# Kernel tuning notes

Hardware: AMD Instinct MI355X
Metric: run time of the kernel (lower is better)

Reference implementation:

```python
import jax, jax.numpy as jnp
import numpy as np

B, S, D_IN, D_ATT = 8, 2048, 512, 512

def setup_inputs() -> dict:
    key = jax.random.key(0)
    ks = jax.random.split(key, 7)
    sc = 1.0 / np.sqrt(D_IN)
    return {
        "x": jax.random.normal(ks[0], (B, S, D_IN), dtype=jnp.float32),
        "Wq": jax.random.uniform(ks[1], (D_IN, D_ATT), jnp.float32, -sc, sc),
        "bq": jax.random.uniform(ks[2], (D_ATT,), jnp.float32, -sc, sc),
        "Wk": jax.random.uniform(ks[3], (D_IN, D_ATT), jnp.float32, -sc, sc),
        "bk": jax.random.uniform(ks[4], (D_ATT,), jnp.float32, -sc, sc),
        "Wv": jax.random.uniform(ks[5], (D_IN, D_ATT), jnp.float32, -sc, sc),
        "bv": jax.random.uniform(ks[6], (D_ATT,), jnp.float32, -sc, sc),
    }

def reference(x, Wq, bq, Wk, bk, Wv, bv):
    # Linear projections: [B, S, D_att]
    q = jnp.einsum("bsd,de->bse", x, Wq) + bq
    k = jnp.einsum("bsd,de->bse", x, Wk) + bk
    v = jnp.einsum("bsd,de->bse", x, Wv) + bv
    # Full scores matrix [B, S, S]; note: NO 1/sqrt(d) scaling in original.
    scores = jnp.einsum("bqe,bke->bqk", q, k)
    attn = jax.nn.softmax(scores, axis=-1)
    return jnp.einsum("bqk,bke->bqe", attn, v)
```

## Files before the change

### kernel.cpp

```cpp
#include <hip/hip_runtime.h>
#include <cstdint>
#include <cstddef>


#define SEQ 2048
#define DIM 512
#define NB 8
#define BSZ (NB * SEQ)
#define KT 64
#define NT (SEQ / KT)

typedef __attribute__((ext_vector_type(8))) _Float16 half8;
typedef __attribute__((ext_vector_type(4))) float f32x4;

__device__ __forceinline__ unsigned short f2h(float f) {
  _Float16 h = (_Float16)f;
  return __builtin_bit_cast(unsigned short, h);
}
__device__ __forceinline__ half8 ld_frag(const unsigned short* p) {
  return *(const half8*)(const void*)p;
}
__device__ __forceinline__ void gl_lds16(const unsigned short* g, unsigned short* l) {
  __builtin_amdgcn_global_load_lds(
      (__attribute__((address_space(1))) void*)g,
      (__attribute__((address_space(3))) void*)l, 16, 0, 0);
}
__device__ __forceinline__ void bar_vm0() {
  asm volatile("s_waitcnt vmcnt(0)\ns_barrier" ::: "memory");
}
__device__ __forceinline__ void bar_lgkm_vm0() {
  asm volatile("s_waitcnt lgkmcnt(0) vmcnt(0)\ns_barrier" ::: "memory");
}

__global__ __launch_bounds__(256) void cvt_x_kernel(
    const float* __restrict__ X, unsigned short* __restrict__ xh)
{
  size_t i0 = ((size_t)blockIdx.x * 256 + threadIdx.x) * 8;
  float4 a = *(const float4*)&X[i0];
  float4 b = *(const float4*)&X[i0 + 4];
  ushort4 o0; o0.x = f2h(a.x); o0.y = f2h(a.y); o0.z = f2h(a.z); o0.w = f2h(a.w);
  ushort4 o1; o1.x = f2h(b.x); o1.y = f2h(b.y); o1.z = f2h(b.z); o1.w = f2h(b.w);
  *(ushort4*)&xh[i0] = o0;
  *(ushort4*)&xh[i0 + 4] = o1;
}

__global__ __launch_bounds__(256) void cvt_w_kernel(
    const float* __restrict__ Wq, const float* __restrict__ Wk,
    const float* __restrict__ Wv, unsigned short* __restrict__ Wt)
{
  const int z = blockIdx.z;
  const float* W = (z == 0) ? Wq : (z == 1) ? Wk : Wv;
  unsigned short* out = Wt + (size_t)z * DIM * DIM;
  const int k0 = blockIdx.x * 64, n0 = blockIdx.y * 64;
  const int t = threadIdx.x;
  __shared__ unsigned short tl[64 * 72];
#pragma unroll
  for (int i = 0; i < 4; i++) {
    int f = t + 256 * i;
    int kr = f >> 4, c4 = (f & 15) * 4;
    float4 v = *(const float4*)&W[(size_t)(k0 + kr) * DIM + n0 + c4];
    tl[(c4 + 0) * 72 + kr] = f2h(v.x);
    tl[(c4 + 1) * 72 + kr] = f2h(v.y);
    tl[(c4 + 2) * 72 + kr] = f2h(v.z);
    tl[(c4 + 3) * 72 + kr] = f2h(v.w);
  }
  __syncthreads();
#pragma unroll
  for (int i = 0; i < 2; i++) {
    int f = t + 256 * i;
    int nr = f >> 3, k8 = (f & 7) * 8;
    *(uint4*)&out[(size_t)(n0 + nr) * DIM + k0 + k8] = *(const uint4*)&tl[nr * 72 + k8];
  }
}

__global__ __launch_bounds__(256) void proj_kernel(
    const unsigned short* __restrict__ xh, const unsigned short* __restrict__ Wt,
    const float* __restrict__ bq, const float* __restrict__ bk,
    const float* __restrict__ bv, unsigned short* __restrict__ outbase)
{
  const int z = blockIdx.z;
  const unsigned short* Wz = Wt + (size_t)z * DIM * DIM;
  const float* bias = (z == 0) ? bq : (z == 1) ? bk : bv;
  unsigned short* out = outbase + (size_t)z * BSZ * DIM;
  const int m0 = blockIdx.x * 128, n0 = blockIdx.y * 128;
  const int t = threadIdx.x, lane = t & 63, wave = t >> 6;
  const int wrow = (wave >> 1) * 64, wcol = (wave & 1) * 64;
  const int lr = lane & 15, lq = (lane >> 4) * 8;

  __shared__ unsigned short sm[128 * 132];
  unsigned short* As = sm;
  unsigned short* Bs = sm + 128 * 64;

  f32x4 acc[4][4];
  const f32x4 zero = {0.f, 0.f, 0.f, 0.f};
#pragma unroll
  for (int r = 0; r < 4; r++)
#pragma unroll
    for (int c = 0; c < 4; c++) acc[r][c] = zero;

  for (int k0 = 0; k0 < DIM; k0 += 64) {
    __syncthreads();
#pragma unroll
    for (int i = 0; i < 4; i++) {
      int f = t + 256 * i;
      int row = f >> 3, c8 = (f & 7) * 8;
      gl_lds16(&xh[(size_t)(m0 + row) * DIM + k0 + c8], &As[i * 2048 + wave * 512]);
      gl_lds16(&Wz[(size_t)(n0 + row) * DIM + k0 + c8], &Bs[i * 2048 + wave * 512]);
    }
    __syncthreads();
#pragma unroll
    for (int kk = 0; kk < 64; kk += 32) {
      half8 a[4], b[4];
#pragma unroll
      for (int r = 0; r < 4; r++) a[r] = ld_frag(&As[(wrow + 16 * r + lr) * 64 + kk + lq]);
#pragma unroll
      for (int c = 0; c < 4; c++) b[c] = ld_frag(&Bs[(wcol + 16 * c + lr) * 64 + kk + lq]);
#pragma unroll
      for (int r = 0; r < 4; r++)
#pragma unroll
        for (int c = 0; c < 4; c++)
          acc[r][c] = __builtin_amdgcn_mfma_f32_16x16x32_f16(a[r], b[c], acc[r][c], 0, 0, 0);
    }
  }
  __syncthreads();
#pragma unroll
  for (int c = 0; c < 4; c++) {
    float bb = bias[n0 + wcol + 16 * c + lr];
#pragma unroll
    for (int r = 0; r < 4; r++)
#pragma unroll
      for (int e = 0; e < 4; e++)
        sm[(wrow + 16 * r + (lane >> 4) * 4 + e) * 132 + wcol + 16 * c + lr] =
            f2h(acc[r][c][e] + bb);
  }
  __syncthreads();
#pragma unroll
  for (int i = 0; i < 8; i++) {
    int f = t + 256 * i;
    int row = f >> 4, c8 = (f & 15) * 8;
    *(uint4*)&out[(size_t)(m0 + row) * DIM + n0 + c8] = *(const uint4*)&sm[row * 132 + c8];
  }
}

__global__ __launch_bounds__(256) void vtrans_kernel(
    const unsigned short* __restrict__ vh, unsigned short* __restrict__ vt)
{
  const int b = blockIdx.z;
  const int s0 = blockIdx.x * 64, n0 = blockIdx.y * 64;
  const int t = threadIdx.x;
  __shared__ unsigned short tl[64 * 72];
#pragma unroll
  for (int i = 0; i < 2; i++) {
    int f = t + 256 * i;
    int sr = f >> 3, c8 = (f & 7) * 8;
    uint4 raw = *(const uint4*)&vh[((size_t)b * SEQ + s0 + sr) * DIM + n0 + c8];
    unsigned short u[8];
    *(uint4*)u = raw;
#pragma unroll
    for (int j = 0; j < 8; j++) tl[(c8 + j) * 72 + sr] = u[j];
  }
  __syncthreads();
#pragma unroll
  for (int i = 0; i < 2; i++) {
    int f = t + 256 * i;
    int nr = f >> 3, s8 = (f & 7) * 8;
    *(uint4*)&vt[((size_t)b * DIM + n0 + nr) * SEQ + s0 + s8] = *(const uint4*)&tl[nr * 72 + s8];
  }
}

#define PSTR 72
#define OSTR 516

__global__ __launch_bounds__(256, 1) void flash_kernel(
    const unsigned short* __restrict__ Qb, const unsigned short* __restrict__ Kb,
    const unsigned short* __restrict__ Vtb, float* __restrict__ Ob)
{
  const int zb = blockIdx.x & 7;
  const int q0 = (blockIdx.x >> 3) * 64;
  const unsigned short* Q = Qb + (size_t)zb * SEQ * DIM;
  const unsigned short* K = Kb + (size_t)zb * SEQ * DIM;
  const unsigned short* V = Vtb + (size_t)zb * DIM * SEQ;
  float* Out = Ob + (size_t)zb * SEQ * DIM;

  const int t = threadIdx.x, lane = t & 63, wave = t >> 6;
  const int lr = lane & 15, lq4 = lane >> 4;
  const float L2E = 1.4426950408889634f;

  __shared__ unsigned short lds[32768 + 32768 + 64 * PSTR + 128 + 128];
  unsigned short* KbufK = lds;
  unsigned short* KbufV = lds + 32768;
  unsigned short* Pbuf = lds + 65536;
  float* abuf = (float*)(lds + 65536 + 64 * PSTR);
  float* lbuf = abuf + 64;

  int koff[16], voff[16];
#pragma unroll
  for (int i = 0; i < 16; i++) {
    int f = t + 256 * i;
    {
      int row = f >> 6, c = f & 63, gc = c ^ (row & 7);
      koff[i] = row * DIM + gc * 8;
    }
    {
      int row = f >> 3, c = f & 7, gc = c ^ (row & 7);
      voff[i] = row * SEQ + gc * 8;
    }
  }

#pragma unroll
  for (int i = 0; i < 16; i++)
    gl_lds16(&Q[(size_t)q0 * DIM + koff[i]], &KbufK[i * 2048 + wave * 512]);
  bar_vm0();
  half8 qf[16];
  {
    const int qrow = 16 * wave + lr;
#pragma unroll
    for (int j = 0; j < 16; j++)
      qf[j] = ld_frag(&KbufK[qrow * 512 + (((4 * j + lq4) ^ (qrow & 7)) << 3)]);
  }
  __syncthreads();

#pragma unroll
  for (int i = 0; i < 16; i++)
    gl_lds16(&K[koff[i]], &KbufK[i * 2048 + wave * 512]);

  f32x4 acc[32];
  const f32x4 zero = {0.f, 0.f, 0.f, 0.f};
#pragma unroll
  for (int ob = 0; ob < 32; ob++) acc[ob] = zero;
  float m_run[4], l_run[4];
#pragma unroll
  for (int e = 0; e < 4; e++) { m_run[e] = -__builtin_inff(); l_run[e] = 0.f; }

  for (int kt = 0; kt < NT; kt++) {
    bar_vm0();

    {
      const unsigned short* Vt = V + kt * KT;
#pragma unroll
      for (int i = 0; i < 16; i++)
        gl_lds16(&Vt[voff[i]], &KbufV[i * 2048 + wave * 512]);
    }

    f32x4 sacc[4];
#pragma unroll
    for (int c = 0; c < 4; c++) sacc[c] = zero;
#pragma unroll
    for (int j = 0; j < 16; j++) {
#pragma unroll
      for (int c = 0; c < 4; c++) {
        int key = 16 * c + lr;
        half8 bf = ld_frag(&KbufK[key * 512 + (((4 * j + lq4) ^ (key & 7)) << 3)]);
        sacc[c] = __builtin_amdgcn_mfma_f32_16x16x32_f16(qf[j], bf, sacc[c], 0, 0, 0);
      }
    }

#pragma unroll
    for (int e = 0; e < 4; e++) {
      float mx = fmaxf(fmaxf(sacc[0][e], sacc[1][e]), fmaxf(sacc[2][e], sacc[3][e]));
      mx = fmaxf(mx, __shfl_xor(mx, 1, 64));
      mx = fmaxf(mx, __shfl_xor(mx, 2, 64));
      mx = fmaxf(mx, __shfl_xor(mx, 4, 64));
      mx = fmaxf(mx, __shfl_xor(mx, 8, 64));
      float mnew = fmaxf(m_run[e], mx);
      float alpha = exp2f((m_run[e] - mnew) * L2E);
      m_run[e] = mnew;
      float sum = 0.f;
#pragma unroll
      for (int c = 0; c < 4; c++) {
        float p = exp2f((sacc[c][e] - mnew) * L2E);
        sum += p;
        Pbuf[(wave * 16 + lq4 * 4 + e) * PSTR + 16 * c + lr] = f2h(p);
      }
      sum += __shfl_xor(sum, 1, 64);
      sum += __shfl_xor(sum, 2, 64);
      sum += __shfl_xor(sum, 4, 64);
      sum += __shfl_xor(sum, 8, 64);
      l_run[e] = alpha * l_run[e] + sum;
      if (lr == 0) abuf[wave * 16 + lq4 * 4 + e] = alpha;
    }

    bar_lgkm_vm0();

    if (kt + 1 < NT) {
      const unsigned short* Kt = K + (size_t)(kt + 1) * KT * DIM;
#pragma unroll
      for (int i = 0; i < 16; i++)
        gl_lds16(&Kt[koff[i]], &KbufK[i * 2048 + wave * 512]);
    }

#pragma unroll
    for (int rg = 0; rg < 4; rg++)
#pragma unroll
      for (int e = 0; e < 4; e++) {
        float a = abuf[rg * 16 + lq4 * 4 + e];
#pragma unroll
        for (int dc = 0; dc < 8; dc++) acc[rg * 8 + dc][e] *= a;
      }

    half8 pf[4][2];
#pragma unroll
    for (int rg = 0; rg < 4; rg++)
#pragma unroll
      for (int ks = 0; ks < 2; ks++)
        pf[rg][ks] = ld_frag(&Pbuf[(rg * 16 + lr) * PSTR + ks * 32 + lq4 * 8]);
#pragma unroll
    for (int dc = 0; dc < 8; dc++) {
      int drow = wave * 128 + 16 * dc + lr;
      half8 vf0 = ld_frag(&KbufV[drow * 64 + ((lq4 ^ (drow & 7)) << 3)]);
      half8 vf1 = ld_frag(&KbufV[drow * 64 + (((4 + lq4) ^ (drow & 7)) << 3)]);
#pragma unroll
      for (int rg = 0; rg < 4; rg++) {
        acc[rg * 8 + dc] =
            __builtin_amdgcn_mfma_f32_16x16x32_f16(pf[rg][0], vf0, acc[rg * 8 + dc], 0, 0, 0);
        acc[rg * 8 + dc] =
            __builtin_amdgcn_mfma_f32_16x16x32_f16(pf[rg][1], vf1, acc[rg * 8 + dc], 0, 0, 0);
      }
    }
  }

  if (lr == 0) {
#pragma unroll
    for (int e = 0; e < 4; e++) lbuf[wave * 16 + lq4 * 4 + e] = l_run[e];
  }
  __syncthreads();
  float linv[4][4];
#pragma unroll
  for (int rg = 0; rg < 4; rg++)
#pragma unroll
    for (int e = 0; e < 4; e++) linv[rg][e] = 1.0f / lbuf[rg * 16 + lq4 * 4 + e];

  float* Obuf = (float*)lds;
#pragma unroll
  for (int h = 0; h < 2; h++) {
    __syncthreads();
#pragma unroll
    for (int r2 = 0; r2 < 2; r2++) {
      int rg = h * 2 + r2;
#pragma unroll
      for (int e = 0; e < 4; e++) {
        int rowh = r2 * 16 + lq4 * 4 + e;
#pragma unroll
        for (int dc = 0; dc < 8; dc++)
          Obuf[rowh * OSTR + wave * 128 + dc * 16 + lr] = acc[rg * 8 + dc][e] * linv[rg][e];
      }
    }
    __syncthreads();
#pragma unroll
    for (int i = 0; i < 16; i++) {
      int f = t + 256 * i;
      int rowh = f >> 7, c4 = (f & 127) * 4;
      *(float4*)&Out[(size_t)(q0 + h * 32 + rowh) * DIM + c4] =
          *(const float4*)&Obuf[rowh * OSTR + c4];
    }
  }
}

extern "C" void kernel_launch(void* const* d_in, const int* in_sizes, int n_in,
                              void* d_out, int out_size, void* d_ws, size_t ws_size,
                              hipStream_t stream)
{
  const float* X  = (const float*)d_in[0];
  const float* Wq = (const float*)d_in[1];
  const float* bq = (const float*)d_in[2];
  const float* Wk = (const float*)d_in[3];
  const float* bk = (const float*)d_in[4];
  const float* Wv = (const float*)d_in[5];
  const float* bv = (const float*)d_in[6];
  float* Out = (float*)d_out;

  char* ws = (char*)d_ws;
  const size_t MB = 1u << 20;
  unsigned short* qh = (unsigned short*)(ws);
  unsigned short* kh = (unsigned short*)(ws + 16 * MB);
  unsigned short* vh = (unsigned short*)(ws + 32 * MB);
  unsigned short* vt = (unsigned short*)(ws + 48 * MB);
  unsigned short* xh = (unsigned short*)(ws + 48 * MB);
  unsigned short* Wt = (unsigned short*)(ws + 64 * MB);

  cvt_x_kernel<<<dim3(BSZ * DIM / 2048), 256, 0, stream>>>(X, xh);
  cvt_w_kernel<<<dim3(8, 8, 3), 256, 0, stream>>>(Wq, Wk, Wv, Wt);
  proj_kernel<<<dim3(BSZ / 128, DIM / 128, 3), 256, 0, stream>>>(
      xh, Wt, bq, bk, bv, qh);
  vtrans_kernel<<<dim3(SEQ / 64, DIM / 64, NB), 256, 0, stream>>>(vh, vt);
  flash_kernel<<<dim3(NB * SEQ / 64), 256, 0, stream>>>(qh, kh, vt, Out);
}
```

Before: 310.8 us.

## Double-buffer K in LDS, load V directly to registers, use 32x32 MFMA for QK

Restructures the flash attention loop. K tiles are double-buffered in LDS, and V fragments are loaded straight from global memory into registers instead of being staged through LDS. The QK^T product now uses 32x32x16 MFMAs, with waves split into key and row halves, so the row max and row sum are combined across wave pairs through LDS with extra barriers. The aim is to overlap K prefetch with compute and drop the V LDS staging, at the cost of more barriers, uncoalesced direct V loads, and higher register pressure (qf[32], vf[16]).

```diff
diff --git a/kernel.cpp b/kernel.cpp
--- a/kernel.cpp
+++ b/kernel.cpp
@@ -11,7 +11,9 @@
 #define NT (SEQ / KT)
 
 typedef __attribute__((ext_vector_type(8))) _Float16 half8;
+typedef __attribute__((ext_vector_type(2))) __fp16 fp16x2;
 typedef __attribute__((ext_vector_type(4))) float f32x4;
+typedef __attribute__((ext_vector_type(16))) float f32x16;
 
 __device__ __forceinline__ unsigned short f2h(float f) {
   _Float16 h = (_Float16)f;
@@ -27,6 +29,9 @@
 }
 __device__ __forceinline__ void bar_vm0() {
   asm volatile("s_waitcnt vmcnt(0)\ns_barrier" ::: "memory");
+}
+__device__ __forceinline__ void bar_lgkm() {
+  asm volatile("s_waitcnt lgkmcnt(0)\ns_barrier" ::: "memory");
 }
 __device__ __forceinline__ void bar_lgkm_vm0() {
   asm volatile("s_waitcnt lgkmcnt(0) vmcnt(0)\ns_barrier" ::: "memory");
@@ -183,110 +188,120 @@
   float* Out = Ob + (size_t)zb * SEQ * DIM;
 
   const int t = threadIdx.x, lane = t & 63, wave = t >> 6;
+  const int l31 = lane & 31, hi = lane >> 5;
+  const int kh = wave & 1, rh = wave >> 1;
   const int lr = lane & 15, lq4 = lane >> 4;
   const float L2E = 1.4426950408889634f;
 
-  __shared__ unsigned short lds[32768 + 32768 + 64 * PSTR + 128 + 128];
-  unsigned short* KbufK = lds;
-  unsigned short* KbufV = lds + 32768;
+  __shared__ unsigned short lds[70912];
+  unsigned short* KA = lds;
+  unsigned short* KB = lds + 32768;
   unsigned short* Pbuf = lds + 65536;
-  float* abuf = (float*)(lds + 65536 + 64 * PSTR);
-  float* lbuf = abuf + 64;
-
-  int koff[16], voff[16];
+  float* mpart = (float*)(lds + 65536 + 64 * PSTR);
+  float* lpart = mpart + 128;
+  float* abuf = lpart + 128;
+  float* lrun = abuf + 64;
+
+  if (t < 64) lrun[t] = 0.f;
+
+  int koff[16];
 #pragma unroll
   for (int i = 0; i < 16; i++) {
     int f = t + 256 * i;
-    {
-      int row = f >> 6, c = f & 63, gc = c ^ (row & 7);
-      koff[i] = row * DIM + gc * 8;
-    }
-    {
-      int row = f >> 3, c = f & 7, gc = c ^ (row & 7);
-      voff[i] = row * SEQ + gc * 8;
-    }
+    int row = f >> 6, c = f & 63;
+    koff[i] = row * DIM + (c ^ (row & 7)) * 8;
   }
 
 #pragma unroll
   for (int i = 0; i < 16; i++)
-    gl_lds16(&Q[(size_t)q0 * DIM + koff[i]], &KbufK[i * 2048 + wave * 512]);
-  bar_vm0();
-  half8 qf[16];
+    gl_lds16(&Q[(size_t)q0 * DIM + koff[i]], &KA[i * 2048 + wave * 512]);
+  bar_lgkm_vm0();
+  half8 qf[32];
   {
-    const int qrow = 16 * wave + lr;
-#pragma unroll
-    for (int j = 0; j < 16; j++)
-      qf[j] = ld_frag(&KbufK[qrow * 512 + (((4 * j + lq4) ^ (qrow & 7)) << 3)]);
+    const int qrow = rh * 32 + l31;
+    const int qsw = qrow & 7;
+#pragma unroll
+    for (int j = 0; j < 32; j++)
+      qf[j] = ld_frag(&KA[qrow * 512 + (((2 * j + hi) ^ qsw) << 3)]);
   }
   __syncthreads();
 
 #pragma unroll
   for (int i = 0; i < 16; i++)
-    gl_lds16(&K[koff[i]], &KbufK[i * 2048 + wave * 512]);
+    gl_lds16(&K[koff[i]], &KA[i * 2048 + wave * 512]);
 
   f32x4 acc[32];
   const f32x4 zero = {0.f, 0.f, 0.f, 0.f};
 #pragma unroll
   for (int ob = 0; ob < 32; ob++) acc[ob] = zero;
-  float m_run[4], l_run[4];
-#pragma unroll
-  for (int e = 0; e < 4; e++) { m_run[e] = -__builtin_inff(); l_run[e] = 0.f; }
+  float m_run = -__builtin_inff();
+
+  const unsigned short* cur = KA;
+  unsigned short* nxt = KB;
 
   for (int kt = 0; kt < NT; kt++) {
     bar_vm0();
 
+    half8 vf[16];
     {
-      const unsigned short* Vt = V + kt * KT;
-#pragma unroll
-      for (int i = 0; i < 16; i++)
-        gl_lds16(&Vt[voff[i]], &KbufV[i * 2048 + wave * 512]);
-    }
-
-    f32x4 sacc[4];
-#pragma unroll
-    for (int c = 0; c < 4; c++) sacc[c] = zero;
-#pragma unroll
-    for (int j = 0; j < 16; j++) {
-#pragma unroll
-      for (int c = 0; c < 4; c++) {
-        int key = 16 * c + lr;
-        half8 bf = ld_frag(&KbufK[key * 512 + (((4 * j + lq4) ^ (key & 7)) << 3)]);
-        sacc[c] = __builtin_amdgcn_mfma_f32_16x16x32_f16(qf[j], bf, sacc[c], 0, 0, 0);
-      }
-    }
-
-#pragma unroll
-    for (int e = 0; e < 4; e++) {
-      float mx = fmaxf(fmaxf(sacc[0][e], sacc[1][e]), fmaxf(sacc[2][e], sacc[3][e]));
-      mx = fmaxf(mx, __shfl_xor(mx, 1, 64));
-      mx = fmaxf(mx, __shfl_xor(mx, 2, 64));
-      mx = fmaxf(mx, __shfl_xor(mx, 4, 64));
-      mx = fmaxf(mx, __shfl_xor(mx, 8, 64));
-      float mnew = fmaxf(m_run[e], mx);
-      float alpha = exp2f((m_run[e] - mnew) * L2E);
-      m_run[e] = mnew;
-      float sum = 0.f;
-#pragma unroll
-      for (int c = 0; c < 4; c++) {
-        float p = exp2f((sacc[c][e] - mnew) * L2E);
-        sum += p;
-        Pbuf[(wave * 16 + lq4 * 4 + e) * PSTR + 16 * c + lr] = f2h(p);
-      }
-      sum += __shfl_xor(sum, 1, 64);
-      sum += __shfl_xor(sum, 2, 64);
-      sum += __shfl_xor(sum, 4, 64);
-      sum += __shfl_xor(sum, 8, 64);
-      l_run[e] = alpha * l_run[e] + sum;
-      if (lr == 0) abuf[wave * 16 + lq4 * 4 + e] = alpha;
-    }
-
-    bar_lgkm_vm0();
-
+      const unsigned short* Vb = V + (size_t)(wave * 128 + lr) * SEQ + kt * KT + lq4 * 8;
+#pragma unroll
+      for (int dc = 0; dc < 8; dc++)
+#pragma unroll
+        for (int ks = 0; ks < 2; ks++)
+          vf[dc * 2 + ks] = ld_frag(Vb + (size_t)dc * 16 * SEQ + ks * 32);
+    }
     if (kt + 1 < NT) {
       const unsigned short* Kt = K + (size_t)(kt + 1) * KT * DIM;
 #pragma unroll
       for (int i = 0; i < 16; i++)
-        gl_lds16(&Kt[koff[i]], &KbufK[i * 2048 + wave * 512]);
+        gl_lds16(&Kt[koff[i]], &nxt[i * 2048 + wave * 512]);
+    }
+
+    f32x16 sacc = {0.f, 0.f, 0.f, 0.f, 0.f, 0.f, 0.f, 0.f,
+                   0.f, 0.f, 0.f, 0.f, 0.f, 0.f, 0.f, 0.f};
+    {
+      const int keyrow = kh * 32 + l31;
+      const int ksw = keyrow & 7;
+      const unsigned short* Kc = cur + keyrow * 512;
+#pragma unroll
+      for (int j = 0; j < 32; j++) {
+        half8 kf = ld_frag(&Kc[(((2 * j + hi) ^ ksw) << 3)]);
+        sacc = __builtin_amdgcn_mfma_f32_32x32x16_f16(kf, qf[j], sacc, 0, 0, 0);
+      }
+    }
+
+    float mx = sacc[0];
+#pragma unroll
+    for (int i2 = 1; i2 < 16; i2++) mx = fmaxf(mx, sacc[i2]);
+    mx = fmaxf(mx, __shfl_xor(mx, 32, 64));
+    if (lane < 32) mpart[kh * 64 + rh * 32 + lane] = mx;
+    bar_lgkm();
+    float mo = mpart[(kh ^ 1) * 64 + rh * 32 + l31];
+    float mnew = fmaxf(m_run, fmaxf(mx, mo));
+    float alpha = exp2f((m_run - mnew) * L2E);
+    m_run = mnew;
+    if (kh == 0 && lane < 32) abuf[rh * 32 + lane] = alpha;
+    float psum = 0.f;
+    {
+      const int prow = rh * 32 + l31;
+#pragma unroll
+      for (int w = 0; w < 8; w++) {
+        float p0 = exp2f((sacc[2 * w] - mnew) * L2E);
+        float p1 = exp2f((sacc[2 * w + 1] - mnew) * L2E);
+        psum += p0 + p1;
+        fp16x2 pk = __builtin_amdgcn_cvt_pkrtz(p0, p1);
+        int keyoff = (w >> 1) * 8 + (w & 1) * 2 + 4 * hi;
+        *(unsigned int*)&Pbuf[prow * PSTR + kh * 32 + keyoff] =
+            __builtin_bit_cast(unsigned int, pk);
+      }
+    }
+    psum += __shfl_xor(psum, 32, 64);
+    if (lane < 32) lpart[kh * 64 + rh * 32 + lane] = psum;
+    bar_lgkm();
+    if (kh == 0 && lane < 32) {
+      int r = rh * 32 + lane;
+      lrun[r] = alpha * lrun[r] + lpart[r] + lpart[64 + r];
     }
 
 #pragma unroll
@@ -305,30 +320,27 @@
       for (int ks = 0; ks < 2; ks++)
         pf[rg][ks] = ld_frag(&Pbuf[(rg * 16 + lr) * PSTR + ks * 32 + lq4 * 8]);
 #pragma unroll
-    for (int dc = 0; dc < 8; dc++) {
-      int drow = wave * 128 + 16 * dc + lr;
-      half8 vf0 = ld_frag(&KbufV[drow * 64 + ((lq4 ^ (drow & 7)) << 3)]);
-      half8 vf1 = ld_frag(&KbufV[drow * 64 + (((4 + lq4) ^ (drow & 7)) << 3)]);
+    for (int dc = 0; dc < 8; dc++)
 #pragma unroll
       for (int rg = 0; rg < 4; rg++) {
         acc[rg * 8 + dc] =
-            __builtin_amdgcn_mfma_f32_16x16x32_f16(pf[rg][0], vf0, acc[rg * 8 + dc], 0, 0, 0);
+            __builtin_amdgcn_mfma_f32_16x16x32_f16(pf[rg][0], vf[dc * 2 + 0],
+                                                   acc[rg * 8 + dc], 0, 0, 0);
         acc[rg * 8 + dc] =
-            __builtin_amdgcn_mfma_f32_16x16x32_f16(pf[rg][1], vf1, acc[rg * 8 + dc], 0, 0, 0);
-      }
-    }
-  }
-
-  if (lr == 0) {
-#pragma unroll
-    for (int e = 0; e < 4; e++) lbuf[wave * 16 + lq4 * 4 + e] = l_run[e];
-  }
-  __syncthreads();
+            __builtin_amdgcn_mfma_f32_16x16x32_f16(pf[rg][1], vf[dc * 2 + 1],
+                                                   acc[rg * 8 + dc], 0, 0, 0);
+      }
+
+    { const unsigned short* tmp = cur; cur = nxt; nxt = (unsigned short*)tmp; }
+  }
+
+  bar_lgkm_vm0();
+
   float linv[4][4];
 #pragma unroll
   for (int rg = 0; rg < 4; rg++)
 #pragma unroll
-    for (int e = 0; e < 4; e++) linv[rg][e] = 1.0f / lbuf[rg * 16 + lq4 * 4 + e];
+    for (int e = 0; e < 4; e++) linv[rg][e] = 1.0f / lrun[rg * 16 + lq4 * 4 + e];
 
   float* Obuf = (float*)lds;
 #pragma unroll
```

Result: slower. 399.1 us (+28.4%).
